# Optimization experiments

Measured on AMD Instinct MI355X. Metric: run time of the kernel, lower is better.

Reference implementation:

```python
import jax, jax.numpy as jnp
import numpy as np

# All unordered pairs of 6 ligand sites (octahedral complex)
PAIRS = np.array([(i, j) for i in range(6) for j in range(i + 1, 6)], dtype=np.int32)  # [15, 2]

B, N_LIGS, D = 32768, 6, 64
IN_DIM = D + 2 * D  # core + lig_i + lig_j = 192
H1, H2 = 64, 32


def setup_inputs() -> dict:
    key = jax.random.key(0)
    ks = jax.random.split(key, 8)
    s = 0.05  # small init scale for numerical sanity
    return {
        "core": jax.random.normal(ks[0], (B, D), dtype=jnp.float32),
        "ligs": jax.random.normal(ks[1], (B, N_LIGS, D), dtype=jnp.float32),
        "W1": jax.random.normal(ks[2], (IN_DIM, H1), dtype=jnp.float32) * s,
        "b1": jnp.zeros((H1,), dtype=jnp.float32),
        "W2": jax.random.normal(ks[3], (H1, H2), dtype=jnp.float32) * s,
        "b2": jnp.zeros((H2,), dtype=jnp.float32),
        "W3": jax.random.normal(ks[4], (H2, 1), dtype=jnp.float32) * s,
        "b3": jnp.zeros((1,), dtype=jnp.float32),
    }


def _mlp(x, W1, b1, W2, b2, W3, b3):
    # Dense(softplus) -> Dense(softplus) -> Dense(1, linear); dropout is identity at inference
    h = jax.nn.softplus(x @ W1 + b1)
    h = jax.nn.softplus(h @ W2 + b2)
    return h @ W3 + b3  # [..., 1]


def reference(core, ligs, W1, b1, W2, b2, W3, b3):
    i_idx = jnp.asarray(PAIRS[:, 0])
    j_idx = jnp.asarray(PAIRS[:, 1])
    P = PAIRS.shape[0]
    li = ligs[:, i_idx, :]  # [B, P, D]
    lj = ligs[:, j_idx, :]  # [B, P, D]
    c = jnp.broadcast_to(core[:, None, :], (core.shape[0], P, core.shape[1]))
    x1 = jnp.concatenate([c, li, lj], axis=-1)  # [B, P, 3D]
    x2 = jnp.concatenate([c, lj, li], axis=-1)  # [B, P, 3D]
    res = 0.5 * (_mlp(x1, W1, b1, W2, b2, W3, b3) + _mlp(x2, W1, b1, W2, b2, W3, b3))  # [B, P, 1]
    return jnp.sum(res, axis=1)  # [B, 1]
```

## Files before the change

### kernel.cpp

```cpp
#include <hip/hip_runtime.h>
#include <hip/hip_fp16.h>
#include <stdint.h>


typedef __attribute__((ext_vector_type(8))) _Float16 f16x8;
typedef __attribute__((ext_vector_type(2))) __fp16   fp16v2;
typedef __attribute__((ext_vector_type(4))) float    f32x4;
typedef __attribute__((ext_vector_type(4))) unsigned int u32x4;

constexpr int   BPB       = 32;
constexpr int   NT        = 1024;
constexpr int   T_STRIDE  = 1680;
constexpr int   WT_RS     = 72;
constexpr int   WT_OFF    = BPB * T_STRIDE;
constexpr int   Y_OFF     = WT_OFF + 192 * WT_RS * 2;
constexpr int   LDS_BYTES = Y_OFF + 128;

constexpr int   WS_W1T   = 0;
constexpr int   WS_W2T   = 24576;
constexpr int   WS_B1    = 28672;
constexpr int   WS_B2    = 28928;
constexpr int   WS_W3    = 29056;
constexpr int   WS_BYTES = 29184;

constexpr float L2E = 1.4426950408889634f;
constexpr float LN2 = 0.6931471805599453f;

constexpr unsigned long long I_BITS =
  (0ull<<0)|(0ull<<3)|(0ull<<6)|(0ull<<9)|(0ull<<12)|
  (1ull<<15)|(1ull<<18)|(1ull<<21)|(1ull<<24)|
  (2ull<<27)|(2ull<<30)|(2ull<<33)|
  (3ull<<36)|(3ull<<39)|(4ull<<42);
constexpr unsigned long long J_BITS =
  (1ull<<0)|(2ull<<3)|(3ull<<6)|(4ull<<9)|(5ull<<12)|
  (2ull<<15)|(3ull<<18)|(4ull<<21)|(5ull<<24)|
  (3ull<<27)|(4ull<<30)|(5ull<<33)|
  (4ull<<36)|(5ull<<39)|(5ull<<42);

__device__ __forceinline__ float sp2(float s) {
  float t = __builtin_amdgcn_exp2f(s);
  return __builtin_amdgcn_logf(1.0f + t);
}

__device__ __forceinline__ __half2 h1pair(__half2 u, __half2 a, __half2 b,
                                          __half2 one2) {
  __half2 s = __hadd2(__hadd2(u, a), b);
  __half2 t = h2exp2(s);
  return h2log2(__hadd2(one2, t));
}

__global__ __launch_bounds__(256)
void prep(const float* __restrict__ W1, const float* __restrict__ b1,
          const float* __restrict__ W2, const float* __restrict__ b2,
          const float* __restrict__ W3, char* __restrict__ ws)
{
  const int t = (int)(blockIdx.x * blockDim.x + threadIdx.x);
  uint16_t* w1t = (uint16_t*)(ws + WS_W1T);
  uint16_t* w2t = (uint16_t*)(ws + WS_W2T);
  float*    b1s = (float*)(ws + WS_B1);
  float*    b2s = (float*)(ws + WS_B2);
  float*    w3s = (float*)(ws + WS_W3);
  if (t < 12288) {
    const int d = t >> 6, n = t & 63;
    const int slab = d >> 6;
    w1t[(slab * 64 + n) * 64 + (d & 63)] =
        __half_as_ushort(__float2half(W1[t] * L2E));
  } else if (t < 14336) {
    const int e = t - 12288;
    const int k = e >> 5, m = e & 31;
    w2t[m * 64 + k] = __half_as_ushort(__float2half(W2[e]));
  } else if (t < 14400) {
    b1s[t - 14336] = b1[t - 14336] * L2E;
  } else if (t < 14432) {
    b2s[t - 14400] = b2[t - 14400] * L2E;
  } else if (t < 14464) {
    w3s[t - 14432] = W3[t - 14432] * LN2;
  }
}

__global__ __launch_bounds__(NT, 8)
void tb_fused(const float* __restrict__ core, const float* __restrict__ ligs,
              const float* __restrict__ b3,   const char* __restrict__ ws,
              float* __restrict__ out)
{
  extern __shared__ char smem[];
  const int tid  = (int)threadIdx.x;
  const int lane = tid & 63;
  const int ln   = lane & 15;
  const int qd   = lane >> 4;
  const int wv   = __builtin_amdgcn_readfirstlane(tid >> 6);
  const int b0   = (int)blockIdx.x * BPB;

  const uint16_t* w2t = (const uint16_t*)(ws + WS_W2T);
  const float*    b1s = (const float*)(ws + WS_B1);
  const float*    b2s = (const float*)(ws + WS_B2);
  const float*    w3s = (const float*)(ws + WS_W3);

  float* yred = (float*)(smem + Y_OFF);

  #pragma unroll
  for (int rep = 0; rep < 3; ++rep) {
    const int c   = tid + rep * NT;
    const int row = c >> 4, col = c & 15;
    *(uint2*)(smem + WT_OFF + row * (WT_RS * 2) + col * 8) =
        *(const uint2*)(ws + WS_W1T + row * 128 + col * 8);
  }
  if (tid < BPB) yred[tid] = 0.0f;
  __syncthreads();

  if (wv < 14) {
    const int xr = wv >> 1;
    const int mt = wv & 1;
    const float* src = (xr == 0)
        ? (core + (size_t)(b0 + mt * 16 + ln) * 64)
        : (ligs + ((size_t)(b0 + mt * 16 + ln) * 6 + (size_t)(xr - 1)) * 64);

    union AF { f16x8 v; fp16v2 p[4]; } Afr[2];
    #pragma unroll
    for (int ks = 0; ks < 2; ++ks) {
      const float4 f0 = *(const float4*)(src + ks * 32 + qd * 8);
      const float4 f1 = *(const float4*)(src + ks * 32 + qd * 8 + 4);
      Afr[ks].p[0] = __builtin_amdgcn_cvt_pkrtz(f0.x, f0.y);
      Afr[ks].p[1] = __builtin_amdgcn_cvt_pkrtz(f0.z, f0.w);
      Afr[ks].p[2] = __builtin_amdgcn_cvt_pkrtz(f1.x, f1.y);
      Afr[ks].p[3] = __builtin_amdgcn_cvt_pkrtz(f1.z, f1.w);
    }

    const int sl_lo = (xr == 0) ? 0 : 1;
    const int sl_hi = (xr == 0) ? 0 : 2;
    #pragma unroll 1
    for (int sl = sl_lo; sl <= sl_hi; ++sl) {
      const int trow = (xr == 0) ? 0 : ((sl == 1) ? xr : 6 + xr);
      #pragma unroll
      for (int nt = 0; nt < 4; ++nt) {
        f32x4 c = {0.f, 0.f, 0.f, 0.f};
        #pragma unroll
        for (int ks = 0; ks < 2; ++ks) {
          const f16x8 Bf = *(const f16x8*)(smem + WT_OFF +
              ((sl * 64 + nt * 16 + ln) * WT_RS + ks * 32 + qd * 8) * 2);
          c = __builtin_amdgcn_mfma_f32_16x16x32_f16(Afr[ks].v, Bf, c, 0, 0, 0);
        }
        const float bias = (trow == 0) ? b1s[nt * 16 + ln] : 0.0f;
        #pragma unroll
        for (int reg = 0; reg < 4; ++reg) {
          const int b = mt * 16 + qd * 4 + reg;
          *(uint16_t*)(smem + (size_t)b * T_STRIDE + trow * 128 + (nt * 16 + ln) * 2) =
              __half_as_ushort(__float2half(c[reg] + bias));
        }
      }
    }
  }

  f16x8 W2f[2][2];
  #pragma unroll
  for (int nt = 0; nt < 2; ++nt)
    #pragma unroll
    for (int ks = 0; ks < 2; ++ks)
      W2f[nt][ks] = *(const f16x8*)(w2t + (nt * 16 + ln) * 64 + ks * 32 + qd * 8);
  float b2v[2], w3v[2];
  #pragma unroll
  for (int nt = 0; nt < 2; ++nt) {
    b2v[nt] = b2s[nt * 16 + ln];
    w3v[nt] = w3s[nt * 16 + ln];
  }

  __syncthreads();

  const int mtw = wv & 1;
  const int qr  = wv >> 1;
  const __half2 one2 = __float2half2_rn(1.0f);
  const char* Tb  = smem + (size_t)(mtw * 16 + ln) * T_STRIDE;
  const int koff  = qd * 16;

  float yacc[4] = {0.f, 0.f, 0.f, 0.f};

  #pragma unroll 2
  for (int t3 = 0; t3 < 4; ++t3) {
    const int q = qr + 8 * t3;
    if (q >= 30) break;
    const int p  = q >> 1;
    const int iv = (int)((I_BITS >> (3 * p)) & 7ull);
    const int jv = (int)((J_BITS >> (3 * p)) & 7ull);
    const int An = (q & 1) ? jv : iv;
    const int Bn = (q & 1) ? iv : jv;
    const char* TA = Tb + (1 + An) * 128;
    const char* TB = Tb + (7 + Bn) * 128;

    union U4 { u32x4 u; __half2 h[4]; };
    U4 du0, da0, db0, du1, da1, db1;
    du0.u = *(const u32x4*)(Tb + koff);
    da0.u = *(const u32x4*)(TA + koff);
    db0.u = *(const u32x4*)(TB + koff);
    du1.u = *(const u32x4*)(Tb + 64 + koff);
    da1.u = *(const u32x4*)(TA + 64 + koff);
    db1.u = *(const u32x4*)(TB + 64 + koff);

    union { f16x8 v; __half2 h[4]; } A0, A1;
    #pragma unroll
    for (int w = 0; w < 4; ++w) A0.h[w] = h1pair(du0.h[w], da0.h[w], db0.h[w], one2);
    #pragma unroll
    for (int w = 0; w < 4; ++w) A1.h[w] = h1pair(du1.h[w], da1.h[w], db1.h[w], one2);

    f32x4 c0 = {0.f, 0.f, 0.f, 0.f};
    f32x4 c1 = {0.f, 0.f, 0.f, 0.f};
    c0 = __builtin_amdgcn_mfma_f32_16x16x32_f16(A0.v, W2f[0][0], c0, 0, 0, 0);
    c0 = __builtin_amdgcn_mfma_f32_16x16x32_f16(A1.v, W2f[0][1], c0, 0, 0, 0);
    c1 = __builtin_amdgcn_mfma_f32_16x16x32_f16(A0.v, W2f[1][0], c1, 0, 0, 0);
    c1 = __builtin_amdgcn_mfma_f32_16x16x32_f16(A1.v, W2f[1][1], c1, 0, 0, 0);

    #pragma unroll
    for (int reg = 0; reg < 4; ++reg) {
      yacc[reg] += sp2(c0[reg] + b2v[0]) * w3v[0]
                 + sp2(c1[reg] + b2v[1]) * w3v[1];
    }
  }

  #pragma unroll
  for (int reg = 0; reg < 4; ++reg) {
    float v = yacc[reg];
    v += __shfl_xor(v, 1);
    v += __shfl_xor(v, 2);
    v += __shfl_xor(v, 4);
    v += __shfl_xor(v, 8);
    yacc[reg] = v;
  }
  if (ln == 0) {
    #pragma unroll
    for (int reg = 0; reg < 4; ++reg)
      atomicAdd(&yred[mtw * 16 + qd * 4 + reg], yacc[reg]);
  }
  __syncthreads();
  if (tid < BPB) out[b0 + tid] = 0.5f * yred[tid] + 15.0f * b3[0];
}

extern "C" void kernel_launch(void* const* d_in, const int* in_sizes, int n_in,
                              void* d_out, int out_size, void* d_ws, size_t ws_size,
                              hipStream_t stream) {
  const float* core = (const float*)d_in[0];
  const float* ligs = (const float*)d_in[1];
  const float* W1   = (const float*)d_in[2];
  const float* b1   = (const float*)d_in[3];
  const float* W2   = (const float*)d_in[4];
  const float* b2   = (const float*)d_in[5];
  const float* W3   = (const float*)d_in[6];
  const float* b3   = (const float*)d_in[7];
  float* out = (float*)d_out;
  char*  ws  = (char*)d_ws;

  const int B = in_sizes[0] / 64;
  const int grid = B / BPB;

  prep<<<dim3(57), dim3(256), 0, stream>>>(W1, b1, W2, b2, W3, ws);

  (void)hipFuncSetAttribute((const void*)tb_fused,
                            hipFuncAttributeMaxDynamicSharedMemorySize, LDS_BYTES);
  tb_fused<<<dim3(grid), dim3(NT), LDS_BYTES, stream>>>(
      core, ligs, b3, ws, out);
}
```

Before: 127.3 us.

## Fold weight prep into fused kernel, swizzle LDS, prefetch activations early

Removes the separate prep kernel launch. Each block now converts W1, W2 and the biases from fp32 to fp16 itself. The W1 tile and the hidden-activation tile in LDS use an XOR swizzle instead of row padding, which shrinks the row strides and aims to avoid bank conflicts. Activation loads from global memory are issued before the W1 staging so their latency overlaps with it. In exchange every block redundantly reads and converts the weights from fp32 global memory, including a strided, uncoalesced W2 gather.

```diff
diff --git a/kernel.cpp b/kernel.cpp
--- a/kernel.cpp
+++ b/kernel.cpp
@@ -10,18 +10,10 @@
 
 constexpr int   BPB       = 32;
 constexpr int   NT        = 1024;
-constexpr int   T_STRIDE  = 1680;
-constexpr int   WT_RS     = 72;
+constexpr int   T_STRIDE  = 1664;
 constexpr int   WT_OFF    = BPB * T_STRIDE;
-constexpr int   Y_OFF     = WT_OFF + 192 * WT_RS * 2;
+constexpr int   Y_OFF     = WT_OFF + 192 * 128;
 constexpr int   LDS_BYTES = Y_OFF + 128;
-
-constexpr int   WS_W1T   = 0;
-constexpr int   WS_W2T   = 24576;
-constexpr int   WS_B1    = 28672;
-constexpr int   WS_B2    = 28928;
-constexpr int   WS_W3    = 29056;
-constexpr int   WS_BYTES = 29184;
 
 constexpr float L2E = 1.4426950408889634f;
 constexpr float LN2 = 0.6931471805599453f;
@@ -49,38 +41,11 @@
   return h2log2(__hadd2(one2, t));
 }
 
-__global__ __launch_bounds__(256)
-void prep(const float* __restrict__ W1, const float* __restrict__ b1,
-          const float* __restrict__ W2, const float* __restrict__ b2,
-          const float* __restrict__ W3, char* __restrict__ ws)
-{
-  const int t = (int)(blockIdx.x * blockDim.x + threadIdx.x);
-  uint16_t* w1t = (uint16_t*)(ws + WS_W1T);
-  uint16_t* w2t = (uint16_t*)(ws + WS_W2T);
-  float*    b1s = (float*)(ws + WS_B1);
-  float*    b2s = (float*)(ws + WS_B2);
-  float*    w3s = (float*)(ws + WS_W3);
-  if (t < 12288) {
-    const int d = t >> 6, n = t & 63;
-    const int slab = d >> 6;
-    w1t[(slab * 64 + n) * 64 + (d & 63)] =
-        __half_as_ushort(__float2half(W1[t] * L2E));
-  } else if (t < 14336) {
-    const int e = t - 12288;
-    const int k = e >> 5, m = e & 31;
-    w2t[m * 64 + k] = __half_as_ushort(__float2half(W2[e]));
-  } else if (t < 14400) {
-    b1s[t - 14336] = b1[t - 14336] * L2E;
-  } else if (t < 14432) {
-    b2s[t - 14400] = b2[t - 14400] * L2E;
-  } else if (t < 14464) {
-    w3s[t - 14432] = W3[t - 14432] * LN2;
-  }
-}
-
 __global__ __launch_bounds__(NT, 8)
 void tb_fused(const float* __restrict__ core, const float* __restrict__ ligs,
-              const float* __restrict__ b3,   const char* __restrict__ ws,
+              const float* __restrict__ W1,   const float* __restrict__ b1,
+              const float* __restrict__ W2,   const float* __restrict__ b2,
+              const float* __restrict__ W3,   const float* __restrict__ b3,
               float* __restrict__ out)
 {
   extern __shared__ char smem[];
@@ -88,42 +53,50 @@
   const int lane = tid & 63;
   const int ln   = lane & 15;
   const int qd   = lane >> 4;
+  const int swz  = ln & 7;
   const int wv   = __builtin_amdgcn_readfirstlane(tid >> 6);
   const int b0   = (int)blockIdx.x * BPB;
 
-  const uint16_t* w2t = (const uint16_t*)(ws + WS_W2T);
-  const float*    b1s = (const float*)(ws + WS_B1);
-  const float*    b2s = (const float*)(ws + WS_B2);
-  const float*    w3s = (const float*)(ws + WS_W3);
-
   float* yred = (float*)(smem + Y_OFF);
 
-  #pragma unroll
-  for (int rep = 0; rep < 3; ++rep) {
-    const int c   = tid + rep * NT;
-    const int row = c >> 4, col = c & 15;
-    *(uint2*)(smem + WT_OFF + row * (WT_RS * 2) + col * 8) =
-        *(const uint2*)(ws + WS_W1T + row * 128 + col * 8);
-  }
-  if (tid < BPB) yred[tid] = 0.0f;
-  __syncthreads();
-
+  const int xr = wv >> 1;
+  const int mt = wv & 1;
+  float4 fA[4];
   if (wv < 14) {
-    const int xr = wv >> 1;
-    const int mt = wv & 1;
     const float* src = (xr == 0)
         ? (core + (size_t)(b0 + mt * 16 + ln) * 64)
         : (ligs + ((size_t)(b0 + mt * 16 + ln) * 6 + (size_t)(xr - 1)) * 64);
-
+    #pragma unroll
+    for (int ks = 0; ks < 2; ++ks) {
+      fA[ks * 2 + 0] = *(const float4*)(src + ks * 32 + qd * 8);
+      fA[ks * 2 + 1] = *(const float4*)(src + ks * 32 + qd * 8 + 4);
+    }
+  }
+
+  #pragma unroll
+  for (int rep = 0; rep < 6; ++rep) {
+    const int t  = tid + rep * NT;
+    const int n  = t & 63;
+    const int d0 = (t >> 6) << 1;
+    const float g0 = W1[(size_t)d0 * 64 + n] * L2E;
+    const float g1 = W1[(size_t)(d0 + 1) * 64 + n] * L2E;
+    const uint32_t pk = (uint32_t)__half_as_ushort(__float2half(g0))
+                      | ((uint32_t)__half_as_ushort(__float2half(g1)) << 16);
+    const int slab = d0 >> 6, dl = d0 & 63;
+    *(uint32_t*)(smem + WT_OFF + (slab * 64 + n) * 128
+                 + (((dl >> 3) ^ (n & 7)) << 4) + (dl & 7) * 2) = pk;
+  }
+  if (tid < BPB) yred[tid] = 0.0f;
+  __syncthreads();
+
+  if (wv < 14) {
     union AF { f16x8 v; fp16v2 p[4]; } Afr[2];
     #pragma unroll
     for (int ks = 0; ks < 2; ++ks) {
-      const float4 f0 = *(const float4*)(src + ks * 32 + qd * 8);
-      const float4 f1 = *(const float4*)(src + ks * 32 + qd * 8 + 4);
-      Afr[ks].p[0] = __builtin_amdgcn_cvt_pkrtz(f0.x, f0.y);
-      Afr[ks].p[1] = __builtin_amdgcn_cvt_pkrtz(f0.z, f0.w);
-      Afr[ks].p[2] = __builtin_amdgcn_cvt_pkrtz(f1.x, f1.y);
-      Afr[ks].p[3] = __builtin_amdgcn_cvt_pkrtz(f1.z, f1.w);
+      Afr[ks].p[0] = __builtin_amdgcn_cvt_pkrtz(fA[ks*2].x, fA[ks*2].y);
+      Afr[ks].p[1] = __builtin_amdgcn_cvt_pkrtz(fA[ks*2].z, fA[ks*2].w);
+      Afr[ks].p[2] = __builtin_amdgcn_cvt_pkrtz(fA[ks*2+1].x, fA[ks*2+1].y);
+      Afr[ks].p[3] = __builtin_amdgcn_cvt_pkrtz(fA[ks*2+1].z, fA[ks*2+1].w);
     }
 
     const int sl_lo = (xr == 0) ? 0 : 1;
@@ -136,15 +109,16 @@
         f32x4 c = {0.f, 0.f, 0.f, 0.f};
         #pragma unroll
         for (int ks = 0; ks < 2; ++ks) {
-          const f16x8 Bf = *(const f16x8*)(smem + WT_OFF +
-              ((sl * 64 + nt * 16 + ln) * WT_RS + ks * 32 + qd * 8) * 2);
+          const f16x8 Bf = *(const f16x8*)(smem + WT_OFF
+              + (sl * 64 + nt * 16 + ln) * 128 + ((((ks << 2) + qd) ^ swz) << 4));
           c = __builtin_amdgcn_mfma_f32_16x16x32_f16(Afr[ks].v, Bf, c, 0, 0, 0);
         }
-        const float bias = (trow == 0) ? b1s[nt * 16 + ln] : 0.0f;
+        const float bias = (trow == 0) ? b1[nt * 16 + ln] * L2E : 0.0f;
         #pragma unroll
         for (int reg = 0; reg < 4; ++reg) {
           const int b = mt * 16 + qd * 4 + reg;
-          *(uint16_t*)(smem + (size_t)b * T_STRIDE + trow * 128 + (nt * 16 + ln) * 2) =
+          *(uint16_t*)(smem + (size_t)b * T_STRIDE + trow * 128
+              + ((((nt << 1) + (ln >> 3)) ^ (b & 7)) << 4) + (ln & 7) * 2) =
               __half_as_ushort(__float2half(c[reg] + bias));
         }
       }
@@ -153,15 +127,22 @@
 
   f16x8 W2f[2][2];
   #pragma unroll
-  for (int nt = 0; nt < 2; ++nt)
-    #pragma unroll
-    for (int ks = 0; ks < 2; ++ks)
-      W2f[nt][ks] = *(const f16x8*)(w2t + (nt * 16 + ln) * 64 + ks * 32 + qd * 8);
+  for (int nt = 0; nt < 2; ++nt) {
+    #pragma unroll
+    for (int ks = 0; ks < 2; ++ks) {
+      union { f16x8 v; uint16_t u[8]; } w;
+      #pragma unroll
+      for (int j = 0; j < 8; ++j)
+        w.u[j] = __half_as_ushort(__float2half(
+            W2[(size_t)(ks * 32 + qd * 8 + j) * 32 + nt * 16 + ln]));
+      W2f[nt][ks] = w.v;
+    }
+  }
   float b2v[2], w3v[2];
   #pragma unroll
   for (int nt = 0; nt < 2; ++nt) {
-    b2v[nt] = b2s[nt * 16 + ln];
-    w3v[nt] = w3s[nt * 16 + ln];
+    b2v[nt] = b2[nt * 16 + ln] * L2E;
+    w3v[nt] = W3[nt * 16 + ln] * LN2;
   }
 
   __syncthreads();
@@ -169,8 +150,9 @@
   const int mtw = wv & 1;
   const int qr  = wv >> 1;
   const __half2 one2 = __float2half2_rn(1.0f);
-  const char* Tb  = smem + (size_t)(mtw * 16 + ln) * T_STRIDE;
-  const int koff  = qd * 16;
+  const char* Tb = smem + (size_t)(mtw * 16 + ln) * T_STRIDE;
+  const int k0 = ((qd)     ^ swz) << 4;
+  const int k1 = ((qd + 4) ^ swz) << 4;
 
   float yacc[4] = {0.f, 0.f, 0.f, 0.f};
 
@@ -188,12 +170,12 @@
 
     union U4 { u32x4 u; __half2 h[4]; };
     U4 du0, da0, db0, du1, da1, db1;
-    du0.u = *(const u32x4*)(Tb + koff);
-    da0.u = *(const u32x4*)(TA + koff);
-    db0.u = *(const u32x4*)(TB + koff);
-    du1.u = *(const u32x4*)(Tb + 64 + koff);
-    da1.u = *(const u32x4*)(TA + 64 + koff);
-    db1.u = *(const u32x4*)(TB + 64 + koff);
+    du0.u = *(const u32x4*)(Tb + k0);
+    da0.u = *(const u32x4*)(TA + k0);
+    db0.u = *(const u32x4*)(TB + k0);
+    du1.u = *(const u32x4*)(Tb + k1);
+    da1.u = *(const u32x4*)(TA + k1);
+    db1.u = *(const u32x4*)(TB + k1);
 
     union { f16x8 v; __half2 h[4]; } A0, A1;
     #pragma unroll
@@ -236,6 +218,7 @@
 extern "C" void kernel_launch(void* const* d_in, const int* in_sizes, int n_in,
                               void* d_out, int out_size, void* d_ws, size_t ws_size,
                               hipStream_t stream) {
+  (void)d_ws; (void)ws_size;
   const float* core = (const float*)d_in[0];
   const float* ligs = (const float*)d_in[1];
   const float* W1   = (const float*)d_in[2];
@@ -245,15 +228,12 @@
   const float* W3   = (const float*)d_in[6];
   const float* b3   = (const float*)d_in[7];
   float* out = (float*)d_out;
-  char*  ws  = (char*)d_ws;
 
   const int B = in_sizes[0] / 64;
   const int grid = B / BPB;
-
-  prep<<<dim3(57), dim3(256), 0, stream>>>(W1, b1, W2, b2, W3, ws);
 
   (void)hipFuncSetAttribute((const void*)tb_fused,
                             hipFuncAttributeMaxDynamicSharedMemorySize, LDS_BYTES);
   tb_fused<<<dim3(grid), dim3(NT), LDS_BYTES, stream>>>(
-      core, ligs, b3, ws, out);
-}
+      core, ligs, W1, b1, W2, b2, W3, b3, out);
+}
```

New measurement: 127.4 us. No clear change (+0.1%).
